# Kernel optimization log

Hardware: AMD Instinct MI355X
Metric: run time of the kernel (lower is better)

The kernel has to match this reference:

```python
import jax, jax.numpy as jnp
import numpy as np

LAYER_SIZES = [256, 256, 256, 128]
MAX_PATHS = 100
BATCH = 16


def setup_inputs() -> dict:
    key = jax.random.key(0)
    ks = jax.random.split(key, 20)
    d = {}
    d["x"] = jax.random.normal(ks[0], (BATCH, LAYER_SIZES[0]), dtype=jnp.float32)
    # PathPreservingLayer weights W_l: [out, in]
    for l in range(3):
        fi, fo = LAYER_SIZES[l], LAYER_SIZES[l + 1]
        d[f"W{l}"] = jax.random.normal(ks[1 + l], (fo, fi), dtype=jnp.float32) / np.sqrt(fi)
        # quality scorer for layer l: Linear(fo,32) -> ReLU -> Linear(32,1)
        kk = jax.random.split(ks[4 + l], 4)
        d[f"s{l}_w1"] = jax.random.normal(kk[0], (32, fo), dtype=jnp.float32) / np.sqrt(fo)
        d[f"s{l}_b1"] = jnp.zeros((32,), dtype=jnp.float32)
        d[f"s{l}_w2"] = jax.random.normal(kk[1], (1, 32), dtype=jnp.float32) / np.sqrt(32.0)
        d[f"s{l}_b2"] = jnp.zeros((1,), dtype=jnp.float32)
    return d


def _path_layer(data, W):
    # data: [B, Fin, P]; W: [Fout, Fin]
    # path-preserving expansion: new[b, j, p*Fin + i] = W[j, i] * data[b, i, p]
    B, I, P = data.shape
    O = W.shape[0]
    out = jnp.einsum("oi,bip->bopi", W, data)  # [B, O, P, I]
    return out.reshape(B, O, P * I)


def _score(data, w1, b1, w2, b2):
    # data: [B, F, P] -> scores [B, P] via tiny MLP over feature dim per path
    t = jnp.swapaxes(data, 1, 2)  # [B, P, F]
    h = jax.nn.relu(jnp.einsum("bpf,hf->bph", t, w1) + b1)
    return (jnp.einsum("bph,oh->bpo", h, w2) + b2)[..., 0]


def _prune(data, scores, keep):
    _, idx = jax.lax.top_k(scores, keep)  # [B, keep]
    return jnp.take_along_axis(data, idx[:, None, :], axis=-1)


def reference(x, W0, W1, W2,
              s0_w1, s0_b1, s0_w2, s0_b2,
              s1_w1, s1_b1, s1_w2, s1_b2,
              s2_w1, s2_b1, s2_w2, s2_b2):
    Ws = [W0, W1, W2]
    scorers = [(s0_w1, s0_b1, s0_w2, s0_b2),
               (s1_w1, s1_b1, s1_w2, s1_b2),
               (s2_w1, s2_b1, s2_w2, s2_b2)]
    data = x[..., None]  # [B, F0, 1]
    n = len(Ws)
    for i in range(n):
        data = _path_layer(data, Ws[i])
        if data.shape[-1] > MAX_PATHS:
            sc = _score(data, *scorers[i])
            data = _prune(data, sc, MAX_PATHS)
        if i < n - 1:
            data = jnp.tanh(data)
    # quality-weighted output with the last scorer
    w = jax.nn.softmax(_score(data, *scorers[-1]), axis=-1)  # [B, P]
    return jnp.sum(data * w[:, None, :], axis=-1)  # [B, F_last]
```

## Files before the change

kernel.cpp:

```cpp
#include <hip/hip_runtime.h>
#include <math.h>

#define NT 1024
#define KSEL 100
#define NWAVE 16
#define HPAD 260
#define CCAP 2048

#define WS_FLOATS_A 239104
#define WS_FLOATS_B 189952

__device__ __forceinline__ unsigned fkey(float f) {
  unsigned u = __float_as_uint(f);
  return (u & 0x80000000u) ? ~u : (u | 0x80000000u);
}
__device__ __forceinline__ float unfkey(unsigned k) {
  return __uint_as_float((k & 0x80000000u) ? (k & 0x7FFFFFFFu) : ~k);
}
__device__ __forceinline__ unsigned long long lower_mask(int lane) {
  return lane ? (~0ull >> (64 - lane)) : 0ull;
}

__device__ __forceinline__ void scan_step(const unsigned* hb, int ncopies, int lane,
                                          int& krem, unsigned& prefix) {
  const int l4 = lane << 2;
  unsigned h0 = 0, h1 = 0, h2 = 0, h3 = 0;
  #pragma unroll 2
  for (int k = 0; k < ncopies; ++k) {
    const uint4 v = *(const uint4*)&hb[k * HPAD + l4];
    h0 += v.x; h1 += v.y; h2 += v.z; h3 += v.w;
  }
  unsigned csum = h0 + h1 + h2 + h3;
  unsigned S = csum;
  #pragma unroll
  for (int off = 1; off < 64; off <<= 1) {
    unsigned v = __shfl_down(S, off, 64);
    if (lane + off < 64) S += v;
  }
  unsigned tail = S - csum;
  unsigned s3 = tail + h3;
  unsigned s2 = s3 + h2;
  unsigned s1 = s2 + h1;
  unsigned s0v = s1 + h0;
  int ld = -1; unsigned sfx = 0, hd = 0;
  if      ((int)s3  >= krem) { ld = l4 + 3; sfx = s3;  hd = h3; }
  else if ((int)s2  >= krem) { ld = l4 + 2; sfx = s2;  hd = h2; }
  else if ((int)s1  >= krem) { ld = l4 + 1; sfx = s1;  hd = h1; }
  else if ((int)s0v >= krem) { ld = l4 + 0; sfx = s0v; hd = h0; }
  int gd = ld;
  #pragma unroll
  for (int off = 32; off >= 1; off >>= 1) {
    int v = __shfl_down(gd, off, 64);
    if (lane + off < 64) gd = (v > gd) ? v : gd;
  }
  gd = __shfl(gd, 0, 64);
  unsigned osfx = __shfl(sfx, gd >> 2, 64);
  unsigned ohd  = __shfl(hd,  gd >> 2, 64);
  krem -= (int)(osfx - ohd);
  prefix = (prefix << 8) | (unsigned)gd;
}

__global__ __launch_bounds__(256) void pqn_precompute(
    const float* __restrict__ W0, const float* __restrict__ W1, const float* __restrict__ W2,
    const float* __restrict__ s0w1, const float* __restrict__ s1w1, const float* __restrict__ s2w1,
    float* __restrict__ ctp0, float* __restrict__ ctp1,
    float* __restrict__ w0t, float* __restrict__ w1t, float* __restrict__ w2t,
    int split)
{
  __shared__ float tile[64][65];
  const int bx = blockIdx.x, t = threadIdx.x;
  const int ctBlocks = split ? 192 : 96;
  if (bx < ctBlocks) {
    int id = bx * 256 + t;
    int l, half, rr;
    if (split) { l = id >> 14; int r = id & 16383; half = r >> 13; rr = r & 8191; }
    else       { l = id >> 13; half = 0; rr = id & 8191; }
    int h = rr >> 8, i = rr & 255;
    const float* W  = (l == 0) ? W0 : (l == 1) ? W1 : W2;
    const float* w1 = (l == 0) ? s0w1 : (l == 1) ? s1w1 : s2w1;
    float acc = 0.f;
    if (split) {
      if (l == 2) {
        int j0 = half * 64;
        #pragma unroll 32
        for (int j = j0; j < j0 + 64; ++j)  acc = fmaf(w1[h * 128 + j], W[j * 256 + i], acc);
      } else {
        int j0 = half * 128;
        #pragma unroll 32
        for (int j = j0; j < j0 + 128; ++j) acc = fmaf(w1[h * 256 + j], W[j * 256 + i], acc);
      }
      (half ? ctp1 : ctp0)[l * 8192 + h * 256 + i] = acc;
    } else {
      if (l == 2) {
        #pragma unroll 32
        for (int j = 0; j < 128; ++j) acc = fmaf(w1[h * 128 + j], W[j * 256 + i], acc);
      } else {
        #pragma unroll 32
        for (int j = 0; j < 256; ++j) acc = fmaf(w1[h * 256 + j], W[j * 256 + i], acc);
      }
      ctp0[l * 8192 + h * 256 + i] = acc;
    }
  } else {
    int tb = bx - ctBlocks;
    const float* W; float* WT; int R, tbl;
    if (tb < 16)      { W = W0; WT = w0t; R = 256; tbl = tb; }
    else if (tb < 32) { W = W1; WT = w1t; R = 256; tbl = tb - 16; }
    else              { W = W2; WT = w2t; R = 128; tbl = tb - 32; }
    int tr = tbl >> 2, tc = tbl & 3;
    int c = t & 63, r0 = t >> 6;
    #pragma unroll
    for (int k = 0; k < 16; ++k) {
      int r = r0 + (k << 2);
      tile[r][c] = W[(tr * 64 + r) * 256 + tc * 64 + c];
    }
    __syncthreads();
    int r2 = t & 63;
    #pragma unroll
    for (int k = 0; k < 16; ++k) {
      int c2 = r0 + (k << 2);
      WT[(tc * 64 + c2) * R + tr * 64 + r2] = tile[r2][c2];
    }
  }
}

__global__ __launch_bounds__(256) void pqn_ab(
    const float* __restrict__ s0w2, const float* __restrict__ s1w2, const float* __restrict__ s2w2,
    const float* __restrict__ ctp0, const float* __restrict__ ctp1,
    float* __restrict__ ct, float* __restrict__ A, float* __restrict__ B,
    int split)
{
  const int l = blockIdx.x;
  const int i = threadIdx.x;
  const float* w2 = (l == 0) ? s0w2 : (l == 1) ? s1w2 : s2w2;
  float a = 0.f, bn = 0.f;
  #pragma unroll
  for (int h = 0; h < 32; ++h) {
    const int o = l * 8192 + h * 256 + i;
    float c = ctp0[o];
    if (split) { c += ctp1[o]; ct[o] = c; }
    float wc = w2[h] * c;
    if (c > 0.f) a += wc; else if (c < 0.f) bn += wc;
  }
  A[l * 256 + i] = a;
  B[l * 256 + i] = bn;
}

__device__ __forceinline__ float slow_c(const float* __restrict__ w1,
                                        const float* __restrict__ W,
                                        int Fout, int h, int i) {
  float c = 0.f;
  for (int j = 0; j < Fout; ++j) c = fmaf(w1[h * Fout + j], W[j * 256 + i], c);
  return c;
}

__global__ __launch_bounds__(NT) void pqn_main(
    const float* __restrict__ x,
    const float* __restrict__ W0, const float* __restrict__ W1, const float* __restrict__ W2,
    const float* __restrict__ s0w1, const float* __restrict__ s1w1, const float* __restrict__ s2w1,
    const float* __restrict__ s0b1, const float* __restrict__ s1b1, const float* __restrict__ s2b1,
    const float* __restrict__ s0w2, const float* __restrict__ s1w2, const float* __restrict__ s2w2,
    const float* __restrict__ s0b2, const float* __restrict__ s1b2, const float* __restrict__ s2b2,
    const float* __restrict__ Ctg, const float* __restrict__ Ag, const float* __restrict__ Bg,
    const float* __restrict__ W0T, const float* __restrict__ W1T, const float* __restrict__ W2T,
    float* __restrict__ out)
{
  __shared__ __align__(16) unsigned keyLds[25 * NT];
  __shared__ __align__(16) unsigned hist0[NWAVE * HPAD];
  __shared__ __align__(16) unsigned histP[6 * HPAD];
  __shared__ unsigned candK[CCAP]; __shared__ int candE[CCAP];
  __shared__ float Asm[256], Bsm[256];
  __shared__ int   path_col[KSEL]; __shared__ float path_t[KSEL];
  __shared__ int   sel_col[KSEL];  __shared__ float sel_s[KSEL]; __shared__ float sel_sc[KSEL];
  __shared__ unsigned tieq[128];
  __shared__ int nsel_s, ntie_s, ncand_s;
  __shared__ int bz_sh[3];
  __shared__ float wts[KSEL];
  __shared__ float partial[8][128];

  const int b = blockIdx.x;
  const int t = threadIdx.x;
  const int lane = t & 63;
  const int w = t >> 6;
  const bool useWs = (Ctg != nullptr);

  if (!useWs) {
    if (t < 256) {
      float a = 0.f, bn = 0.f;
      for (int h = 0; h < 32; ++h) {
        float c = slow_c(s0w1, W0, 256, h, t);
        float wc = s0w2[h] * c;
        if (c > 0.f) a += wc; else if (c < 0.f) bn += wc;
      }
      Asm[t] = a; Bsm[t] = bn;
    }
    __syncthreads();
  }
  if (w == 0) {
    {
      float v0 = (lane < 32) ? s0b1[lane] : 0.f;
      float v1 = (lane < 32) ? s1b1[lane] : 0.f;
      float v2 = (lane < 32) ? s2b1[lane] : 0.f;
      bz_sh[0] = (__ballot(v0 != 0.f) == 0ull);
      bz_sh[1] = (__ballot(v1 != 0.f) == 0ull);
      bz_sh[2] = (__ballot(v2 != 0.f) == 0ull);
    }
    const bool bz0 = (bz_sh[0] != 0);
    const float b2v = s0b2[0];
    const float4 xv4 = *(const float4*)(x + b * 256 + lane * 4);
    const float xv[4] = {xv4.x, xv4.y, xv4.z, xv4.w};
    float4 A4, B4;
    if (useWs) { A4 = *(const float4*)(Ag + lane * 4); B4 = *(const float4*)(Bg + lane * 4); }
    else       { A4 = *(const float4*)(Asm + lane * 4); B4 = *(const float4*)(Bsm + lane * 4); }
    const float Av[4] = {A4.x, A4.y, A4.z, A4.w};
    const float Bv[4] = {B4.x, B4.y, B4.z, B4.w};
    unsigned kq[4];
    #pragma unroll
    for (int q = 0; q < 4; ++q) {
      int e = 4 * lane + q;
      float s = xv[q];
      float v;
      if (bz0) v = s * (s > 0.f ? Av[q] : Bv[q]) + b2v;
      else {
        v = b2v;
        for (int h = 0; h < 32; ++h) {
          float c = useWs ? Ctg[h * 256 + e] : slow_c(s0w1, W0, 256, h, e);
          v += s0w2[h] * fmaxf(fmaf(s, c, s0b1[h]), 0.f);
        }
      }
      kq[q] = fkey(v);
    }
    int krem = KSEL; unsigned prefix = 0u;
    #pragma unroll
    for (int pass = 0; pass < 4; ++pass) {
      unsigned* hw = (pass == 0) ? hist0 : (histP + (pass - 1) * 2 * HPAD);
      const int l4 = lane << 2;
      hw[l4] = 0u; hw[l4 + 1] = 0u; hw[l4 + 2] = 0u; hw[l4 + 3] = 0u;
      const int shift = 24 - 8 * pass;
      #pragma unroll
      for (int q = 0; q < 4; ++q) {
        bool cand = (pass == 0) || ((kq[q] >> (shift + 8)) == prefix);
        if (cand) atomicAdd(&hw[(kq[q] >> shift) & 255u], 1u);
      }
      scan_step(hw, 1, lane, krem, prefix);
    }
    const unsigned T = prefix;
    int total = 0, ttot = 0;
    #pragma unroll
    for (int q = 0; q < 4; ++q) {
      int e = 4 * lane + q;
      bool sel = kq[q] > T;
      unsigned long long m = __ballot(sel);
      if (sel) {
        int slot = total + (int)__popcll(m & lower_mask(lane));
        path_col[slot] = e; path_t[slot] = xv[q];
      }
      total += (int)__popcll(m);
      bool tie = (kq[q] == T);
      unsigned long long tm = __ballot(tie);
      if (tie) {
        int ts = ttot + (int)__popcll(tm & lower_mask(lane));
        if (ts < 128) tieq[ts] = (unsigned)e;
      }
      ttot += (int)__popcll(tm);
    }
    if (lane == 0) {
      int m = ttot > 128 ? 128 : ttot;
      for (int a2 = 1; a2 < m; ++a2) {
        unsigned v = tieq[a2]; int c = a2 - 1;
        while (c >= 0 && tieq[c] > v) { tieq[c + 1] = tieq[c]; --c; }
        tieq[c + 1] = v;
      }
    }
    const int kt = KSEL - total;
    if (lane < kt) {
      int e = (int)tieq[lane];
      path_col[total + lane] = e; path_t[total + lane] = x[b * 256 + e];
    }
  }
  __syncthreads();

  for (int l = 1; l < 3; ++l) {
    const float* w1 = (l == 1) ? s1w1 : s2w1;
    const float* b1 = (l == 1) ? s1b1 : s2b1;
    const float* w2 = (l == 1) ? s1w2 : s2w2;
    const float  b2v = (l == 1) ? s1b2[0] : s2b2[0];
    const float* Wl = (l == 1) ? W1 : W2;
    const float* Wprev = (l == 1) ? W0 : W1;
    const float* WTprev = (l == 1) ? W0T : W1T;
    const int Fout = (l == 2) ? 128 : 256;

    const float* Ap; const float* Bp;
    if (useWs) { Ap = Ag + l * 256; Bp = Bg + l * 256; }
    else {
      if (t < 256) {
        float a = 0.f, bn = 0.f;
        for (int h = 0; h < 32; ++h) {
          float c = slow_c(w1, Wl, Fout, h, t);
          float wc = w2[h] * c;
          if (c > 0.f) a += wc; else if (c < 0.f) bn += wc;
        }
        Asm[t] = a; Bsm[t] = bn;
      }
      __syncthreads();
      Ap = Asm; Bp = Bsm;
    }
    const bool bz = (bz_sh[l] != 0);
    const float* ctp = useWs ? (Ctg + l * 8192) : nullptr;

    const int i = t & 255;
    const int pq = t >> 8;
    const float Ai = Ap[i], Bi = Bp[i];
    unsigned* histw0 = hist0 + w * HPAD;
    {
      const int l4 = lane << 2;
      histw0[l4] = 0u; histw0[l4 + 1] = 0u; histw0[l4 + 2] = 0u; histw0[l4 + 3] = 0u;
    }
    for (int id = t; id < 6 * HPAD; id += NT) histP[id] = 0u;
    if (t == 0) { nsel_s = 0; ntie_s = 0; ncand_s = 0; }
    unsigned runD = 0x100u; unsigned runC = 0u;
    if (useWs && bz) {
      #pragma unroll
      for (int g = 0; g < 25; g += 8) {
        float wv[8], tv[8];
        #pragma unroll
        for (int jj = 0; jj < 8; ++jj) {
          if (g + jj < 25) {
            int p = pq + ((g + jj) << 2);
            tv[jj] = path_t[p];
            wv[jj] = WTprev[(path_col[p] << 8) + i];
          }
        }
        #pragma unroll
        for (int jj = 0; jj < 8; ++jj) {
          if (g + jj < 25) {
            float s = tanhf(wv[jj] * tv[jj]);
            float v = s * (s > 0.f ? Ai : Bi) + b2v;
            unsigned k = fkey(v);
            keyLds[(g + jj) * NT + t] = k;
            unsigned d = k >> 24;
            if (d == runD) ++runC;
            else { if (runC) atomicAdd(&histw0[runD], runC); runD = d; runC = 1u; }
          }
        }
      }
    } else {
      #pragma unroll
      for (int g = 0; g < 25; g += 4) {
        float wv[4];
        #pragma unroll
        for (int jj = 0; jj < 4; ++jj) {
          if (g + jj < 25) {
            int p = pq + ((g + jj) << 2);
            wv[jj] = useWs ? WTprev[(path_col[p] << 8) + i]
                           : Wprev[i * 256 + path_col[p]];
          }
        }
        #pragma unroll
        for (int jj = 0; jj < 4; ++jj) {
          if (g + jj < 25) {
            int p = pq + ((g + jj) << 2);
            float s = tanhf(wv[jj] * path_t[p]);
            float v;
            if (bz) v = s * (s > 0.f ? Ai : Bi) + b2v;
            else {
              v = b2v;
              for (int h = 0; h < 32; ++h) {
                float c = useWs ? ctp[h * 256 + i] : slow_c(w1, Wl, Fout, h, i);
                v += w2[h] * fmaxf(fmaf(s, c, b1[h]), 0.f);
              }
            }
            unsigned k = fkey(v);
            keyLds[(g + jj) * NT + t] = k;
            unsigned d = k >> 24;
            if (d == runD) ++runC;
            else { if (runC) atomicAdd(&histw0[runD], runC); runD = d; runC = 1u; }
          }
        }
      }
    }
    if (runC) atomicAdd(&histw0[runD], runC);

    __syncthreads();
    int krem = KSEL; unsigned prefix = 0u;
    scan_step(hist0, NWAVE, lane, krem, prefix);

    {
      unsigned* hn = histP + (w & 1) * HPAD;
      #pragma unroll
      for (int j = 0; j < 25; ++j) {
        unsigned k = keyLds[j * NT + t];
        if ((k >> 24) == prefix) atomicAdd(&hn[(k >> 16) & 255u], 1u);
      }
    }
    __syncthreads();
    scan_step(histP, 2, lane, krem, prefix);

    {
      unsigned* hn = histP + 2 * HPAD + (w & 1) * HPAD;
      #pragma unroll
      for (int j = 0; j < 25; ++j) {
        unsigned k = keyLds[j * NT + t];
        unsigned p16 = k >> 16;
        if (p16 > prefix) {
          int slot = atomicAdd(&nsel_s, 1);
          int e = j * NT + t; int p = e >> 8;
          float wq = useWs ? WTprev[(path_col[p] << 8) + i] : Wprev[i * 256 + path_col[p]];
          sel_col[slot] = i; sel_s[slot] = tanhf(wq * path_t[p]); sel_sc[slot] = unfkey(k);
        } else if (p16 == prefix) {
          int ci = atomicAdd(&ncand_s, 1);
          if (ci < CCAP) { candK[ci] = k; candE[ci] = j * NT + t; }
          atomicAdd(&hn[(k >> 8) & 255u], 1u);
        }
      }
    }
    __syncthreads();
    scan_step(histP + 2 * HPAD, 2, lane, krem, prefix);
    const int ncand = ncand_s;
    const bool ovf = (ncand > CCAP);

    {
      unsigned* hn = histP + 4 * HPAD + (w & 1) * HPAD;
      if (!ovf) {
        for (int idx = t; idx < ncand; idx += NT) {
          unsigned k = candK[idx];
          if ((k >> 8) == prefix) atomicAdd(&hn[k & 255u], 1u);
        }
      } else {
        #pragma unroll
        for (int j = 0; j < 25; ++j) {
          unsigned k = keyLds[j * NT + t];
          if ((k >> 8) == prefix) atomicAdd(&hn[k & 255u], 1u);
        }
      }
    }
    __syncthreads();
    scan_step(histP + 4 * HPAD, 2, lane, krem, prefix);
    const unsigned T = prefix;

    if (!ovf) {
      for (int idx = t; idx < ncand; idx += NT) {
        unsigned k = candK[idx];
        if (k > T) {
          int e = candE[idx];
          int slot = atomicAdd(&nsel_s, 1);
          int ii = e & 255, p = e >> 8;
          float wq = useWs ? WTprev[(path_col[p] << 8) + ii] : Wprev[ii * 256 + path_col[p]];
          sel_col[slot] = ii; sel_s[slot] = tanhf(wq * path_t[p]); sel_sc[slot] = unfkey(k);
        } else if (k == T) {
          int tp = atomicAdd(&ntie_s, 1);
          if (tp < 128) tieq[tp] = (unsigned)candE[idx];
        }
      }
    } else {
      #pragma unroll
      for (int j = 0; j < 25; ++j) {
        unsigned k = keyLds[j * NT + t];
        if ((k >> 16) == (T >> 16)) {
          int e = j * NT + t;
          if (k > T) {
            int slot = atomicAdd(&nsel_s, 1);
            int p = e >> 8;
            float wq = useWs ? WTprev[(path_col[p] << 8) + i] : Wprev[i * 256 + path_col[p]];
            sel_col[slot] = i; sel_s[slot] = tanhf(wq * path_t[p]); sel_sc[slot] = unfkey(k);
          } else if (k == T) {
            int tp = atomicAdd(&ntie_s, 1);
            if (tp < 128) tieq[tp] = (unsigned)e;
          }
        }
      }
    }
    __syncthreads();

    if (w == 0) {
      const int G = nsel_s;
      const int kt = KSEL - G;
      if (lane == 0 && kt > 1) {
        int m = ntie_s > 128 ? 128 : ntie_s;
        for (int a2 = 1; a2 < m; ++a2) {
          unsigned v = tieq[a2]; int c = a2 - 1;
          while (c >= 0 && tieq[c] > v) { tieq[c + 1] = tieq[c]; --c; }
          tieq[c + 1] = v;
        }
      }
      if (lane < kt) {
        int e = (int)tieq[lane];
        int ii = e & 255, p = e >> 8;
        float wq = useWs ? WTprev[(path_col[p] << 8) + ii] : Wprev[ii * 256 + path_col[p]];
        sel_col[G + lane] = ii;
        sel_s[G + lane] = tanhf(wq * path_t[p]);
        sel_sc[G + lane] = unfkey(T);
      }
      if (l < 2) {
        if (lane < 64) {
          path_col[lane] = sel_col[lane]; path_t[lane] = sel_s[lane];
          if (lane < 36) { path_col[64 + lane] = sel_col[64 + lane]; path_t[64 + lane] = sel_s[64 + lane]; }
        }
      }
    }
    __syncthreads();
  }

  if (w == 0) {
    float s1v = sel_sc[lane];
    float s2v = (lane < 36) ? sel_sc[64 + lane] : -INFINITY;
    float m = fmaxf(s1v, s2v);
    #pragma unroll
    for (int off = 32; off >= 1; off >>= 1) m = fmaxf(m, __shfl_xor(m, off, 64));
    float e1 = expf(s1v - m);
    float e2 = (lane < 36) ? expf(s2v - m) : 0.f;
    float sv = e1 + e2;
    #pragma unroll
    for (int off = 32; off >= 1; off >>= 1) sv += __shfl_xor(sv, off, 64);
    wts[lane] = e1 * sel_s[lane] / sv;
    if (lane < 36) wts[64 + lane] = e2 * sel_s[64 + lane] / sv;
  }
  __syncthreads();
  {
    const int chunk = w >> 1, half = w & 1;
    const int o = half * 64 + lane;
    const int pb = chunk * 13;
    const int pe = (pb + 13 < KSEL) ? pb + 13 : KSEL;
    float acc = 0.f;
    for (int p = pb; p < pe; ++p) {
      float wq = useWs ? W2T[sel_col[p] * 128 + o] : W2[o * 256 + sel_col[p]];
      acc = fmaf(wq, wts[p], acc);
    }
    partial[chunk][o] = acc;
  }
  __syncthreads();
  if (t < 128) {
    float acc = 0.f;
    #pragma unroll
    for (int c = 0; c < 8; ++c) acc += partial[c][t];
    out[b * 128 + t] = acc;
  }
}

extern "C" void kernel_launch(void* const* d_in, const int* in_sizes, int n_in,
                              void* d_out, int out_size, void* d_ws, size_t ws_size,
                              hipStream_t stream) {
  const float* x    = (const float*)d_in[0];
  const float* W0   = (const float*)d_in[1];
  const float* s0w1 = (const float*)d_in[2];
  const float* s0b1 = (const float*)d_in[3];
  const float* s0w2 = (const float*)d_in[4];
  const float* s0b2 = (const float*)d_in[5];
  const float* W1   = (const float*)d_in[6];
  const float* s1w1 = (const float*)d_in[7];
  const float* s1b1 = (const float*)d_in[8];
  const float* s1w2 = (const float*)d_in[9];
  const float* s1b2 = (const float*)d_in[10];
  const float* W2   = (const float*)d_in[11];
  const float* s2w1 = (const float*)d_in[12];
  const float* s2b1 = (const float*)d_in[13];
  const float* s2w2 = (const float*)d_in[14];
  const float* s2b2 = (const float*)d_in[15];
  float* out = (float*)d_out;
  float* ws  = (float*)d_ws;

  const size_t wsf = ws_size / sizeof(float);
  float *ctp0 = nullptr, *ctp1 = nullptr, *ct = nullptr, *A = nullptr, *B = nullptr;
  float *w0t = nullptr, *w1t = nullptr, *w2t = nullptr;
  int split = 0; bool haveWs = false;

  if (wsf >= WS_FLOATS_A) {
    split = 1; haveWs = true;
    ctp0 = ws;            ctp1 = ws + 24576;  ct = ws + 49152;
    A = ws + 73728;       B = ws + 74496;
    w0t = ws + 75264;     w1t = ws + 140800;  w2t = ws + 206336;
  } else if (wsf >= WS_FLOATS_B) {
    split = 0; haveWs = true;
    ct = ws; ctp0 = ws;   ctp1 = nullptr;
    A = ws + 24576;       B = ws + 25344;
    w0t = ws + 26112;     w1t = ws + 91648;   w2t = ws + 157184;
  }

  if (haveWs) {
    pqn_precompute<<<split ? 232 : 136, 256, 0, stream>>>(
        W0, W1, W2, s0w1, s1w1, s2w1, ctp0, ctp1, w0t, w1t, w2t, split);
    pqn_ab<<<3, 256, 0, stream>>>(s0w2, s1w2, s2w2, ctp0, ctp1, ct, A, B, split);
  }
  pqn_main<<<16, NT, 0, stream>>>(x, W0, W1, W2,
                                  s0w1, s1w1, s2w1,
                                  s0b1, s1b1, s2b1,
                                  s0w2, s1w2, s2w2,
                                  s0b2, s1b2, s2b2,
                                  haveWs ? ct : nullptr, A, B, w0t, w1t, w2t,
                                  out);
}
```

Before: 153.0 us.

## Fuse precompute and main kernels into one cooperative launch with grid sync

```diff
diff --git a/kernel.cpp b/kernel.cpp
--- a/kernel.cpp
+++ b/kernel.cpp
@@ -1,5 +1,8 @@
 #include <hip/hip_runtime.h>
+#include <hip/hip_cooperative_groups.h>
 #include <math.h>
+
+namespace cg = cooperative_groups;
 
 #define NT 1024
 #define KSEL 100
@@ -7,8 +10,15 @@
 #define HPAD 260
 #define CCAP 2048
 
-#define WS_FLOATS_A 239104
-#define WS_FLOATS_B 189952
+#define OFF_CT   0
+#define OFF_W0T  24576
+#define OFF_W1T  90112
+#define OFF_W2T  155648
+#define WS_FLOATS 188416
+
+#define NMAIN 16
+#define NCT   24
+#define GRID  34
 
 __device__ __forceinline__ unsigned fkey(float f) {
   unsigned u = __float_as_uint(f);
@@ -60,91 +70,6 @@
   prefix = (prefix << 8) | (unsigned)gd;
 }
 
-__global__ __launch_bounds__(256) void pqn_precompute(
-    const float* __restrict__ W0, const float* __restrict__ W1, const float* __restrict__ W2,
-    const float* __restrict__ s0w1, const float* __restrict__ s1w1, const float* __restrict__ s2w1,
-    float* __restrict__ ctp0, float* __restrict__ ctp1,
-    float* __restrict__ w0t, float* __restrict__ w1t, float* __restrict__ w2t,
-    int split)
-{
-  __shared__ float tile[64][65];
-  const int bx = blockIdx.x, t = threadIdx.x;
-  const int ctBlocks = split ? 192 : 96;
-  if (bx < ctBlocks) {
-    int id = bx * 256 + t;
-    int l, half, rr;
-    if (split) { l = id >> 14; int r = id & 16383; half = r >> 13; rr = r & 8191; }
-    else       { l = id >> 13; half = 0; rr = id & 8191; }
-    int h = rr >> 8, i = rr & 255;
-    const float* W  = (l == 0) ? W0 : (l == 1) ? W1 : W2;
-    const float* w1 = (l == 0) ? s0w1 : (l == 1) ? s1w1 : s2w1;
-    float acc = 0.f;
-    if (split) {
-      if (l == 2) {
-        int j0 = half * 64;
-        #pragma unroll 32
-        for (int j = j0; j < j0 + 64; ++j)  acc = fmaf(w1[h * 128 + j], W[j * 256 + i], acc);
-      } else {
-        int j0 = half * 128;
-        #pragma unroll 32
-        for (int j = j0; j < j0 + 128; ++j) acc = fmaf(w1[h * 256 + j], W[j * 256 + i], acc);
-      }
-      (half ? ctp1 : ctp0)[l * 8192 + h * 256 + i] = acc;
-    } else {
-      if (l == 2) {
-        #pragma unroll 32
-        for (int j = 0; j < 128; ++j) acc = fmaf(w1[h * 128 + j], W[j * 256 + i], acc);
-      } else {
-        #pragma unroll 32
-        for (int j = 0; j < 256; ++j) acc = fmaf(w1[h * 256 + j], W[j * 256 + i], acc);
-      }
-      ctp0[l * 8192 + h * 256 + i] = acc;
-    }
-  } else {
-    int tb = bx - ctBlocks;
-    const float* W; float* WT; int R, tbl;
-    if (tb < 16)      { W = W0; WT = w0t; R = 256; tbl = tb; }
-    else if (tb < 32) { W = W1; WT = w1t; R = 256; tbl = tb - 16; }
-    else              { W = W2; WT = w2t; R = 128; tbl = tb - 32; }
-    int tr = tbl >> 2, tc = tbl & 3;
-    int c = t & 63, r0 = t >> 6;
-    #pragma unroll
-    for (int k = 0; k < 16; ++k) {
-      int r = r0 + (k << 2);
-      tile[r][c] = W[(tr * 64 + r) * 256 + tc * 64 + c];
-    }
-    __syncthreads();
-    int r2 = t & 63;
-    #pragma unroll
-    for (int k = 0; k < 16; ++k) {
-      int c2 = r0 + (k << 2);
-      WT[(tc * 64 + c2) * R + tr * 64 + r2] = tile[r2][c2];
-    }
-  }
-}
-
-__global__ __launch_bounds__(256) void pqn_ab(
-    const float* __restrict__ s0w2, const float* __restrict__ s1w2, const float* __restrict__ s2w2,
-    const float* __restrict__ ctp0, const float* __restrict__ ctp1,
-    float* __restrict__ ct, float* __restrict__ A, float* __restrict__ B,
-    int split)
-{
-  const int l = blockIdx.x;
-  const int i = threadIdx.x;
-  const float* w2 = (l == 0) ? s0w2 : (l == 1) ? s1w2 : s2w2;
-  float a = 0.f, bn = 0.f;
-  #pragma unroll
-  for (int h = 0; h < 32; ++h) {
-    const int o = l * 8192 + h * 256 + i;
-    float c = ctp0[o];
-    if (split) { c += ctp1[o]; ct[o] = c; }
-    float wc = w2[h] * c;
-    if (c > 0.f) a += wc; else if (c < 0.f) bn += wc;
-  }
-  A[l * 256 + i] = a;
-  B[l * 256 + i] = bn;
-}
-
 __device__ __forceinline__ float slow_c(const float* __restrict__ w1,
                                         const float* __restrict__ W,
                                         int Fout, int h, int i) {
@@ -153,22 +78,23 @@
   return c;
 }
 
-__global__ __launch_bounds__(NT) void pqn_main(
+__global__ __launch_bounds__(NT) void pqn_all(
     const float* __restrict__ x,
     const float* __restrict__ W0, const float* __restrict__ W1, const float* __restrict__ W2,
     const float* __restrict__ s0w1, const float* __restrict__ s1w1, const float* __restrict__ s2w1,
     const float* __restrict__ s0b1, const float* __restrict__ s1b1, const float* __restrict__ s2b1,
     const float* __restrict__ s0w2, const float* __restrict__ s1w2, const float* __restrict__ s2w2,
     const float* __restrict__ s0b2, const float* __restrict__ s1b2, const float* __restrict__ s2b2,
-    const float* __restrict__ Ctg, const float* __restrict__ Ag, const float* __restrict__ Bg,
-    const float* __restrict__ W0T, const float* __restrict__ W1T, const float* __restrict__ W2T,
-    float* __restrict__ out)
+    float* __restrict__ wsr,
+    float* __restrict__ out,
+    int doPre)
 {
   __shared__ __align__(16) unsigned keyLds[25 * NT];
   __shared__ __align__(16) unsigned hist0[NWAVE * HPAD];
   __shared__ __align__(16) unsigned histP[6 * HPAD];
   __shared__ unsigned candK[CCAP]; __shared__ int candE[CCAP];
-  __shared__ float Asm[256], Bsm[256];
+  __shared__ __align__(16) float As[3][256];
+  __shared__ __align__(16) float Bs[3][256];
   __shared__ int   path_col[KSEL]; __shared__ float path_t[KSEL];
   __shared__ int   sel_col[KSEL];  __shared__ float sel_s[KSEL]; __shared__ float sel_sc[KSEL];
   __shared__ unsigned tieq[128];
@@ -177,40 +103,102 @@
   __shared__ float wts[KSEL];
   __shared__ float partial[8][128];
 
-  const int b = blockIdx.x;
+  const int bx = blockIdx.x;
   const int t = threadIdx.x;
   const int lane = t & 63;
   const int w = t >> 6;
-  const bool useWs = (Ctg != nullptr);
-
-  if (!useWs) {
-    if (t < 256) {
-      float a = 0.f, bn = 0.f;
+  const bool useWs = (wsr != nullptr);
+
+  if (doPre) {
+    if (bx < NCT) {
+      int id = bx * NT + t;
+      int l = id >> 13, r = id & 8191;
+      int h = r >> 8, i = r & 255;
+      const float* W  = (l == 0) ? W0 : (l == 1) ? W1 : W2;
+      const float* w1 = (l == 0) ? s0w1 : (l == 1) ? s1w1 : s2w1;
+      float acc = 0.f;
+      if (l == 2) {
+        #pragma unroll 32
+        for (int j = 0; j < 128; ++j) acc = fmaf(w1[h * 128 + j], W[j * 256 + i], acc);
+      } else {
+        #pragma unroll 32
+        for (int j = 0; j < 256; ++j) acc = fmaf(w1[h * 256 + j], W[j * 256 + i], acc);
+      }
+      wsr[OFF_CT + l * 8192 + h * 256 + i] = acc;
+    } else {
+      float* tileB = ((float*)keyLds) + (t >> 8) * (64 * 65);
+      const int tt = t & 255;
+      int tb = (bx - NCT) * 4 + (t >> 8);
+      const float* W; float* WT; int R, tbl;
+      if (tb < 16)      { W = W0; WT = wsr + OFF_W0T; R = 256; tbl = tb; }
+      else if (tb < 32) { W = W1; WT = wsr + OFF_W1T; R = 256; tbl = tb - 16; }
+      else              { W = W2; WT = wsr + OFF_W2T; R = 128; tbl = tb - 32; }
+      int tr = tbl >> 2, tc = tbl & 3;
+      int c = tt & 63, r0 = tt >> 6;
+      #pragma unroll
+      for (int k = 0; k < 16; ++k) {
+        int r = r0 + (k << 2);
+        tileB[r * 65 + c] = W[(tr * 64 + r) * 256 + tc * 64 + c];
+      }
+      __syncthreads();
+      int r2 = tt & 63;
+      #pragma unroll
+      for (int k = 0; k < 16; ++k) {
+        int c2 = r0 + (k << 2);
+        WT[(tc * 64 + c2) * R + tr * 64 + r2] = tileB[r2 * 65 + c2];
+      }
+    }
+    cg::this_grid().sync();
+    if (bx >= NMAIN) return;
+  }
+
+  const float* Ctg = useWs ? (wsr + OFF_CT) : nullptr;
+  const float* W0T = useWs ? (wsr + OFF_W0T) : nullptr;
+  const float* W1T = useWs ? (wsr + OFF_W1T) : nullptr;
+  const float* W2T = useWs ? (wsr + OFF_W2T) : nullptr;
+  const int b = bx;
+
+  if (t < 768) {
+    int l = t >> 8, i = t & 255;
+    const float* w2 = (l == 0) ? s0w2 : (l == 1) ? s1w2 : s2w2;
+    float a = 0.f, bn = 0.f;
+    if (useWs) {
+      const float* ct = Ctg + l * 8192;
+      #pragma unroll
       for (int h = 0; h < 32; ++h) {
-        float c = slow_c(s0w1, W0, 256, h, t);
-        float wc = s0w2[h] * c;
+        float c = ct[h * 256 + i];
+        float wc = w2[h] * c;
         if (c > 0.f) a += wc; else if (c < 0.f) bn += wc;
       }
-      Asm[t] = a; Bsm[t] = bn;
-    }
-    __syncthreads();
+    } else {
+      const float* W  = (l == 0) ? W0 : (l == 1) ? W1 : W2;
+      const float* w1 = (l == 0) ? s0w1 : (l == 1) ? s1w1 : s2w1;
+      const int Fout = (l == 2) ? 128 : 256;
+      for (int h = 0; h < 32; ++h) {
+        float c = slow_c(w1, W, Fout, h, i);
+        float wc = w2[h] * c;
+        if (c > 0.f) a += wc; else if (c < 0.f) bn += wc;
+      }
+    }
+    As[l][i] = a; Bs[l][i] = bn;
   }
   if (w == 0) {
-    {
-      float v0 = (lane < 32) ? s0b1[lane] : 0.f;
-      float v1 = (lane < 32) ? s1b1[lane] : 0.f;
-      float v2 = (lane < 32) ? s2b1[lane] : 0.f;
-      bz_sh[0] = (__ballot(v0 != 0.f) == 0ull);
-      bz_sh[1] = (__ballot(v1 != 0.f) == 0ull);
-      bz_sh[2] = (__ballot(v2 != 0.f) == 0ull);
-    }
+    float v0 = (lane < 32) ? s0b1[lane] : 0.f;
+    float v1 = (lane < 32) ? s1b1[lane] : 0.f;
+    float v2 = (lane < 32) ? s2b1[lane] : 0.f;
+    bz_sh[0] = (__ballot(v0 != 0.f) == 0ull);
+    bz_sh[1] = (__ballot(v1 != 0.f) == 0ull);
+    bz_sh[2] = (__ballot(v2 != 0.f) == 0ull);
+  }
+  __syncthreads();
+
+  if (w == 0) {
     const bool bz0 = (bz_sh[0] != 0);
     const float b2v = s0b2[0];
     const float4 xv4 = *(const float4*)(x + b * 256 + lane * 4);
     const float xv[4] = {xv4.x, xv4.y, xv4.z, xv4.w};
-    float4 A4, B4;
-    if (useWs) { A4 = *(const float4*)(Ag + lane * 4); B4 = *(const float4*)(Bg + lane * 4); }
-    else       { A4 = *(const float4*)(Asm + lane * 4); B4 = *(const float4*)(Bsm + lane * 4); }
+    const float4 A4 = *(const float4*)(&As[0][lane * 4]);
+    const float4 B4 = *(const float4*)(&Bs[0][lane * 4]);
     const float Av[4] = {A4.x, A4.y, A4.z, A4.w};
     const float Bv[4] = {B4.x, B4.y, B4.z, B4.w};
     unsigned kq[4];
@@ -288,28 +276,12 @@
     const float* Wprev = (l == 1) ? W0 : W1;
     const float* WTprev = (l == 1) ? W0T : W1T;
     const int Fout = (l == 2) ? 128 : 256;
-
-    const float* Ap; const float* Bp;
-    if (useWs) { Ap = Ag + l * 256; Bp = Bg + l * 256; }
-    else {
-      if (t < 256) {
-        float a = 0.f, bn = 0.f;
-        for (int h = 0; h < 32; ++h) {
-          float c = slow_c(w1, Wl, Fout, h, t);
-          float wc = w2[h] * c;
-          if (c > 0.f) a += wc; else if (c < 0.f) bn += wc;
-        }
-        Asm[t] = a; Bsm[t] = bn;
-      }
-      __syncthreads();
-      Ap = Asm; Bp = Bsm;
-    }
     const bool bz = (bz_sh[l] != 0);
     const float* ctp = useWs ? (Ctg + l * 8192) : nullptr;
 
     const int i = t & 255;
     const int pq = t >> 8;
-    const float Ai = Ap[i], Bi = Bp[i];
+    const float Ai = As[l][i], Bi = Bs[l][i];
     unsigned* histw0 = hist0 + w * HPAD;
     {
       const int l4 = lane << 2;
@@ -558,33 +530,24 @@
   float* out = (float*)d_out;
   float* ws  = (float*)d_ws;
 
-  const size_t wsf = ws_size / sizeof(float);
-  float *ctp0 = nullptr, *ctp1 = nullptr, *ct = nullptr, *A = nullptr, *B = nullptr;
-  float *w0t = nullptr, *w1t = nullptr, *w2t = nullptr;
-  int split = 0; bool haveWs = false;
-
-  if (wsf >= WS_FLOATS_A) {
-    split = 1; haveWs = true;
-    ctp0 = ws;            ctp1 = ws + 24576;  ct = ws + 49152;
-    A = ws + 73728;       B = ws + 74496;
-    w0t = ws + 75264;     w1t = ws + 140800;  w2t = ws + 206336;
-  } else if (wsf >= WS_FLOATS_B) {
-    split = 0; haveWs = true;
-    ct = ws; ctp0 = ws;   ctp1 = nullptr;
-    A = ws + 24576;       B = ws + 25344;
-    w0t = ws + 26112;     w1t = ws + 91648;   w2t = ws + 157184;
-  }
-
-  if (haveWs) {
-    pqn_precompute<<<split ? 232 : 136, 256, 0, stream>>>(
-        W0, W1, W2, s0w1, s1w1, s2w1, ctp0, ctp1, w0t, w1t, w2t, split);
-    pqn_ab<<<3, 256, 0, stream>>>(s0w2, s1w2, s2w2, ctp0, ctp1, ct, A, B, split);
-  }
-  pqn_main<<<16, NT, 0, stream>>>(x, W0, W1, W2,
-                                  s0w1, s1w1, s2w1,
-                                  s0b1, s1b1, s2b1,
-                                  s0w2, s1w2, s2w2,
-                                  s0b2, s1b2, s2b2,
-                                  haveWs ? ct : nullptr, A, B, w0t, w1t, w2t,
-                                  out);
-}
+  if (ws_size >= (size_t)WS_FLOATS * sizeof(float)) {
+    float* wsr = ws; int doPre = 1;
+    void* args[] = {
+      (void*)&x, (void*)&W0, (void*)&W1, (void*)&W2,
+      (void*)&s0w1, (void*)&s1w1, (void*)&s2w1,
+      (void*)&s0b1, (void*)&s1b1, (void*)&s2b1,
+      (void*)&s0w2, (void*)&s1w2, (void*)&s2w2,
+      (void*)&s0b2, (void*)&s1b2, (void*)&s2b2,
+      (void*)&wsr, (void*)&out, (void*)&doPre
+    };
+    hipLaunchCooperativeKernel((const void*)pqn_all, dim3(GRID), dim3(NT),
+                               args, 0, stream);
+  } else {
+    pqn_all<<<NMAIN, NT, 0, stream>>>(x, W0, W1, W2,
+                                      s0w1, s1w1, s2w1,
+                                      s0b1, s1b1, s2b1,
+                                      s0w2, s1w2, s2w2,
+                                      s0b2, s1b2, s2b2,
+                                      nullptr, out, 0);
+  }
+}
```

Result: slower. 197.7 us (+29.2%).
